# Kernel optimization log

Measured on AMD Instinct MI355X. Metric: run time of the kernel, lower is better.

Reference implementation:

```python
import jax, jax.numpy as jnp
import numpy as np

B, L, M = 64, 2048, 128  # trees, leaves per complete binary tree, mem_dim (== in_dim)


def setup_inputs() -> dict:
    key = jax.random.key(0)
    ks = jax.random.split(key, 16)
    n = lambda k, s, sc=1.0: jax.random.normal(k, s, dtype=jnp.float32) * sc
    W = 0.08  # small init scale for gate weights
    return {
        "embs": n(ks[0], (B, L, M)),
        "root_c": n(ks[1], (B, M)),
        "root_h": n(ks[2], (B, M)),
        "Wi": n(ks[3], (M, M), W), "bi": jnp.zeros((M,), jnp.float32),
        "Wf": n(ks[4], (M, M), W), "bf": jnp.zeros((M,), jnp.float32),
        "Wu": n(ks[5], (M, M), W), "bu": jnp.zeros((M,), jnp.float32),
        "Wc": n(ks[6], (M, M), W), "bc": jnp.zeros((M,), jnp.float32),
        "Wo": n(ks[7], (M, M), W), "bo": jnp.zeros((M,), jnp.float32),
    }


def reference(embs, root_c, root_h, Wi, bi, Wf, bf, Wu, bu, Wc, bc, Wo, bo):
    # Top-down binary-tree LSTM over B complete binary trees, vectorized per level.
    Bn, Ln, Mn = embs.shape
    depth = int(np.log2(Ln))  # root at level 0, leaves at level `depth`

    def composer(pc, ph):
        # BinaryTreeTopDownComposer: gates from parent hidden, cell mixes parent cell
        i = jax.nn.sigmoid(ph @ Wi + bi)
        pf = jax.nn.sigmoid(ph @ Wf + bf)
        u = jnp.tanh(ph @ Wu + bu)
        c = i * u + pf * pc
        return c, jnp.tanh(c)

    def leaf(x):
        # BinaryTreeLeafModule
        c = x @ Wc + bc
        o = jax.nn.sigmoid(x @ Wo + bo)
        return c, o * jnp.tanh(c)

    # root state comes from bp_lstm.root_c / root_h
    pc, ph = root_c[:, None, :], root_h[:, None, :]  # [B, 1, M]
    for _ in range(1, depth):  # internal levels: each node composed from its parent
        pc2 = jnp.repeat(pc, 2, axis=1)  # broadcast parent state to both children
        ph2 = jnp.repeat(ph, 2, axis=1)
        pc, ph = composer(pc2, ph2)

    # leaf level: state = cat(leaf(emb), leaf(parent_h), leaf(parent_c)) along features
    pcl = jnp.repeat(pc, 2, axis=1)  # [B, L, M]
    phl = jnp.repeat(ph, 2, axis=1)
    ce, he = leaf(embs)
    cph, hph = leaf(phl)
    cpc, hpc = leaf(pcl)
    c_leaf = jnp.concatenate([ce, cph, cpc], axis=-1)  # [B, L, 3M]
    h_leaf = jnp.concatenate([he, hph, hpc], axis=-1)  # [B, L, 3M]
    return jnp.concatenate([c_leaf, h_leaf], axis=-1)  # [B, L, 6M]
```

## Files before the change

### kernel.cpp

```cpp
#include <hip/hip_runtime.h>
#include <cstdint>
#include <cstddef>

#define Bb   64
#define Ll   2048
#define Mm   128
#define ROWS (Bb * Ll)
#define OUTC 768
#define LDA  136
#define LDF  132

typedef __attribute__((ext_vector_type(4))) float  f32x4;
typedef __attribute__((ext_vector_type(8))) short  bf16x8;
typedef __attribute__((ext_vector_type(4))) short  short4v;
typedef __bf16 bf16x8b __attribute__((ext_vector_type(8)));

__device__ __forceinline__ float rcp_(float x) {
#if __has_builtin(__builtin_amdgcn_rcpf)
    return __builtin_amdgcn_rcpf(x);
#else
    return 1.0f / x;
#endif
}
__device__ __forceinline__ float sigmoid_(float x) {
    return rcp_(1.0f + __expf(-x));
}
__device__ __forceinline__ float tanh_(float x) {
    float ax = fabsf(x);
    float r  = __expf(-2.0f * ax);
    float t  = (1.0f - r) * rcp_(1.0f + r);
    return x < 0.0f ? -t : t;
}
__device__ __forceinline__ short f2bf(float f) {
    uint32_t u = __builtin_bit_cast(uint32_t, f);
    u = (u + 0x7FFFu + ((u >> 16) & 1u)) >> 16;
    return (short)(u & 0xFFFFu);
}

__device__ __forceinline__ void lds_sync() {
    asm volatile("s_waitcnt lgkmcnt(0)\n\ts_barrier" ::: "memory");
}


__global__ __launch_bounds__(512)
void state_kernel(const float* __restrict__ root_c, const float* __restrict__ root_h,
                  const float* __restrict__ Wi, const float* __restrict__ bi,
                  const float* __restrict__ Wf, const float* __restrict__ bfv,
                  const float* __restrict__ Wu, const float* __restrict__ bu,
                  const float* __restrict__ Wc, const float* __restrict__ bc,
                  const float* __restrict__ Wo, const float* __restrict__ bo,
                  float* __restrict__ ws, short* __restrict__ wbf)
{
    const int b   = blockIdx.x;
    const int tid = threadIdx.x;
    const int m   = tid & 127;
    const int q   = tid >> 7;
    const int k0  = q * 32;

    __shared__ float h_sh[Mm];
    __shared__ float c_sh[Mm];
    __shared__ float part[4][4][Mm];

    {
        int idx  = b * 512 + tid;
        int gate = idx >> 14;
        int col  = (idx >> 7) & 127;
        int k    = idx & 127;
        const float* W = gate ? Wo : Wc;
        wbf[idx] = f2bf(W[k * Mm + col]);
    }

    float wi[32], wf[32], wu[32];
    #pragma unroll
    for (int kk = 0; kk < 32; ++kk) {
        wi[kk] = Wi[(k0 + kk) * Mm + m];
        wf[kk] = Wf[(k0 + kk) * Mm + m];
        wu[kk] = Wu[(k0 + kk) * Mm + m];
    }

    float c = 0.f;
    if (q == 0) {
        c = root_c[b * Mm + m];
        h_sh[m] = root_h[b * Mm + m];
    }
    __syncthreads();

    const float bi_m = bi[m], bf_m = bfv[m], bu_m = bu[m];

    for (int it = 0; it < 10; ++it) {
        float di0 = 0.f, di1 = 0.f, df0 = 0.f, df1 = 0.f, du0 = 0.f, du1 = 0.f;
        #pragma unroll
        for (int kk = 0; kk < 32; kk += 2) {
            float h0 = h_sh[k0 + kk], h1 = h_sh[k0 + kk + 1];
            di0 = fmaf(h0, wi[kk], di0);
            di1 = fmaf(h1, wi[kk + 1], di1);
            df0 = fmaf(h0, wf[kk], df0);
            df1 = fmaf(h1, wf[kk + 1], df1);
            du0 = fmaf(h0, wu[kk], du0);
            du1 = fmaf(h1, wu[kk + 1], du1);
        }
        part[0][q][m] = di0 + di1;
        part[1][q][m] = df0 + df1;
        part[2][q][m] = du0 + du1;
        __syncthreads();
        if (q == 0) {
            float di = (part[0][0][m] + part[0][1][m]) + (part[0][2][m] + part[0][3][m]);
            float df = (part[1][0][m] + part[1][1][m]) + (part[1][2][m] + part[1][3][m]);
            float du = (part[2][0][m] + part[2][1][m]) + (part[2][2][m] + part[2][3][m]);
            float ig = sigmoid_(di + bi_m);
            float fg = sigmoid_(df + bf_m);
            float ug = tanh_(du + bu_m);
            c = ig * ug + fg * c;
            h_sh[m] = tanh_(c);
        }
        __syncthreads();
    }
    if (q == 0) c_sh[m] = c;
    __syncthreads();

    float dch = 0.f, doh = 0.f, dcc = 0.f, doc = 0.f;
    #pragma unroll
    for (int kk = 0; kk < 32; ++kk) {
        int k = k0 + kk;
        float hk = h_sh[k], ck = c_sh[k];
        float wc = Wc[k * Mm + m], wo = Wo[k * Mm + m];
        dch = fmaf(hk, wc, dch);
        doh = fmaf(hk, wo, doh);
        dcc = fmaf(ck, wc, dcc);
        doc = fmaf(ck, wo, doc);
    }
    part[0][q][m] = dch;
    part[1][q][m] = doh;
    part[2][q][m] = dcc;
    part[3][q][m] = doc;
    __syncthreads();
    if (q == 0) {
        float Dch = (part[0][0][m] + part[0][1][m]) + (part[0][2][m] + part[0][3][m]);
        float Doh = (part[1][0][m] + part[1][1][m]) + (part[1][2][m] + part[1][3][m]);
        float Dcc = (part[2][0][m] + part[2][1][m]) + (part[2][2][m] + part[2][3][m]);
        float Doc = (part[3][0][m] + part[3][1][m]) + (part[3][2][m] + part[3][3][m]);
        const float bcm = bc[m], bom = bo[m];
        float cph = Dch + bcm;
        float cpc = Dcc + bcm;
        float hph = sigmoid_(Doh + bom) * tanh_(cph);
        float hpc = sigmoid_(Doc + bom) * tanh_(cpc);
        ws[0 * Bb * Mm + b * Mm + m] = cph;
        ws[1 * Bb * Mm + b * Mm + m] = cpc;
        ws[2 * Bb * Mm + b * Mm + m] = hph;
        ws[3 * Bb * Mm + b * Mm + m] = hpc;
    }
}

__global__ __launch_bounds__(512, 4)
void fused_kernel(const float* __restrict__ embs,
                  const short* __restrict__ wbf,
                  const float* __restrict__ bc, const float* __restrict__ bo,
                  const float* __restrict__ state,
                  float* __restrict__ out)
{
    __shared__ __align__(16) char smem[70656];
    short* A0   = (short*)smem;
    short* A1   = (short*)(smem + 17408);
    float* ce_l = (float*)(smem + 34816);
    float* he_l = (float*)(smem + 51712);
    float* st_l = (float*)(smem + 68608);

    const int tid  = threadIdx.x;
    const int w    = tid >> 6;
    const int lane = tid & 63;
    const int g    = lane >> 4;
    const int ln   = lane & 15;
    const int n0   = w * 16 + ln;
    const int rowbase0 = blockIdx.x * 128;
    const int rowbase1 = rowbase0 + 64;
    const int b        = rowbase0 >> 11;

    bf16x8 bfrag[2][4];
    #pragma unroll
    for (int gate = 0; gate < 2; ++gate)
        #pragma unroll
        for (int ks = 0; ks < 4; ++ks)
            bfrag[gate][ks] = *(const bf16x8*)(
                wbf + gate * (Mm * Mm) + n0 * Mm + ks * 32 + g * 8);
    const float biasc = bc[n0];
    const float biaso = bo[n0];
    st_l[tid] = state[(tid >> 7) * (Bb * Mm) + b * Mm + (tid & 127)];

    auto stage_load = [&](int rowbase, f32x4 (&r)[4]) {
        #pragma unroll
        for (int i = 0; i < 4; ++i) {
            int idx = tid + 512 * i;
            int rr  = idx >> 5;
            int kq  = idx & 31;
            r[i] = __builtin_nontemporal_load(
                (const f32x4*)(embs + (size_t)(rowbase + rr) * Mm + kq * 4));
        }
    };
    auto stage_write = [&](short* A, const f32x4 (&r)[4]) {
        #pragma unroll
        for (int i = 0; i < 4; ++i) {
            int idx = tid + 512 * i;
            int rr  = idx >> 5;
            int kq  = idx & 31;
            short4v s4;
            s4[0] = f2bf(r[i][0]); s4[1] = f2bf(r[i][1]);
            s4[2] = f2bf(r[i][2]); s4[3] = f2bf(r[i][3]);
            *(short4v*)(&A[rr * LDA + kq * 4]) = s4;
        }
    };
    auto do_mfma = [&](const short* A, f32x4 (&acc)[4][2]) {
        #pragma unroll
        for (int rt = 0; rt < 4; ++rt)
            #pragma unroll
            for (int gate = 0; gate < 2; ++gate) {
                float bv = gate ? biaso : biasc;
                acc[rt][gate][0] = bv; acc[rt][gate][1] = bv;
                acc[rt][gate][2] = bv; acc[rt][gate][3] = bv;
            }
        #pragma unroll
        for (int ks = 0; ks < 4; ++ks) {
            bf16x8 af[4];
            #pragma unroll
            for (int rt = 0; rt < 4; ++rt)
                af[rt] = *(const bf16x8*)(&A[(rt * 16 + ln) * LDA + ks * 32 + g * 8]);
            #pragma unroll
            for (int rt = 0; rt < 4; ++rt)
                #pragma unroll
                for (int gate = 0; gate < 2; ++gate)
                    acc[rt][gate] = __builtin_amdgcn_mfma_f32_16x16x32_bf16(
                        __builtin_bit_cast(bf16x8b, af[rt]),
                        __builtin_bit_cast(bf16x8b, bfrag[gate][ks]),
                        acc[rt][gate], 0, 0, 0);
        }
    };
    auto epilogue = [&](int rowbase, f32x4 (&acc)[4][2]) {
        #pragma unroll
        for (int half = 0; half < 2; ++half) {
            #pragma unroll
            for (int qq = 0; qq < 2; ++qq) {
                int rt = half * 2 + qq;
                #pragma unroll
                for (int r = 0; r < 4; ++r) {
                    int rowL = qq * 16 + g * 4 + r;
                    float cv = acc[rt][0][r];
                    float hv = sigmoid_(acc[rt][1][r]) * tanh_(cv);
                    ce_l[rowL * LDF + n0] = cv;
                    he_l[rowL * LDF + n0] = hv;
                }
            }
            lds_sync();
            #pragma unroll
            for (int i = 0; i < 12; ++i) {
                int u  = tid + 512 * i;
                int rg = u / 192;
                int s  = u - rg * 192;
                int sec = s >> 5;
                int cc  = s & 31;
                const float* src =
                    (sec == 0) ? (ce_l + rg * LDF + cc * 4) :
                    (sec == 3) ? (he_l + rg * LDF + cc * 4) :
                    (st_l + ((sec < 3) ? (sec - 1) : (sec - 2)) * 128 + cc * 4);
                f32x4 v = *(const f32x4*)src;
                *(f32x4*)(out + (size_t)(rowbase + half * 32 + rg) * OUTC + s * 4) = v;
            }
            lds_sync();
        }
    };

    f32x4 r0[4], r1[4];
    f32x4 acc[4][2];

    stage_load(rowbase0, r0);
    stage_write(A0, r0);
    lds_sync();

    stage_load(rowbase1, r1);

    do_mfma(A0, acc);
    stage_write(A1, r1);
    lds_sync();

    epilogue(rowbase0, acc);
    do_mfma(A1, acc);
    epilogue(rowbase1, acc);
}

extern "C" void kernel_launch(void* const* d_in, const int* in_sizes, int n_in,
                              void* d_out, int out_size, void* d_ws, size_t ws_size,
                              hipStream_t stream) {
    const float* embs   = (const float*)d_in[0];
    const float* root_c = (const float*)d_in[1];
    const float* root_h = (const float*)d_in[2];
    const float* Wi = (const float*)d_in[3];
    const float* bi = (const float*)d_in[4];
    const float* Wf = (const float*)d_in[5];
    const float* bfv= (const float*)d_in[6];
    const float* Wu = (const float*)d_in[7];
    const float* bu = (const float*)d_in[8];
    const float* Wc = (const float*)d_in[9];
    const float* bc = (const float*)d_in[10];
    const float* Wo = (const float*)d_in[11];
    const float* bo = (const float*)d_in[12];

    float* out   = (float*)d_out;
    float* state = (float*)d_ws;
    short* wbf   = (short*)d_ws + 65536;

    state_kernel<<<dim3(Bb), dim3(512), 0, stream>>>(
        root_c, root_h, Wi, bi, Wf, bfv, Wu, bu, Wc, bc, Wo, bo, state, wbf);
    fused_kernel<<<dim3(1024), dim3(512), 0, stream>>>(
        embs, wbf, bc, bo, state, out);
}
```

Before: 110.0 us.

## Load MFMA A-fragments directly from global memory, dropping LDS staging

Replaces the LDS-staged, double-buffered bf16 A tiles with direct per-lane global loads of fp32 embeddings that are converted to bf16 in registers and fed straight into the MFMA. This removes the LDS write/read traffic and one barrier, and cuts shared memory per block, which may allow more resident blocks. In exchange, all 8 waves now load the same A data redundantly from global/L2 (eightfold re-reads), the loads are less coalesced, and the explicit overlap of the next tile's load with the current MFMA is gone.

```diff
diff --git a/kernel.cpp b/kernel.cpp
--- a/kernel.cpp
+++ b/kernel.cpp
@@ -7,12 +7,10 @@
 #define Mm   128
 #define ROWS (Bb * Ll)
 #define OUTC 768
-#define LDA  136
 #define LDF  132
 
 typedef __attribute__((ext_vector_type(4))) float  f32x4;
 typedef __attribute__((ext_vector_type(8))) short  bf16x8;
-typedef __attribute__((ext_vector_type(4))) short  short4v;
 typedef __bf16 bf16x8b __attribute__((ext_vector_type(8)));
 
 __device__ __forceinline__ float rcp_(float x) {
@@ -158,12 +156,9 @@
                   const float* __restrict__ state,
                   float* __restrict__ out)
 {
-    __shared__ __align__(16) char smem[70656];
-    short* A0   = (short*)smem;
-    short* A1   = (short*)(smem + 17408);
-    float* ce_l = (float*)(smem + 34816);
-    float* he_l = (float*)(smem + 51712);
-    float* st_l = (float*)(smem + 68608);
+    __shared__ float ce_l[32 * LDF];
+    __shared__ float he_l[32 * LDF];
+    __shared__ float st_l[512];
 
     const int tid  = threadIdx.x;
     const int w    = tid >> 6;
@@ -172,7 +167,6 @@
     const int ln   = lane & 15;
     const int n0   = w * 16 + ln;
     const int rowbase0 = blockIdx.x * 128;
-    const int rowbase1 = rowbase0 + 64;
     const int b        = rowbase0 >> 11;
 
     bf16x8 bfrag[2][4];
@@ -186,53 +180,6 @@
     const float biaso = bo[n0];
     st_l[tid] = state[(tid >> 7) * (Bb * Mm) + b * Mm + (tid & 127)];
 
-    auto stage_load = [&](int rowbase, f32x4 (&r)[4]) {
-        #pragma unroll
-        for (int i = 0; i < 4; ++i) {
-            int idx = tid + 512 * i;
-            int rr  = idx >> 5;
-            int kq  = idx & 31;
-            r[i] = __builtin_nontemporal_load(
-                (const f32x4*)(embs + (size_t)(rowbase + rr) * Mm + kq * 4));
-        }
-    };
-    auto stage_write = [&](short* A, const f32x4 (&r)[4]) {
-        #pragma unroll
-        for (int i = 0; i < 4; ++i) {
-            int idx = tid + 512 * i;
-            int rr  = idx >> 5;
-            int kq  = idx & 31;
-            short4v s4;
-            s4[0] = f2bf(r[i][0]); s4[1] = f2bf(r[i][1]);
-            s4[2] = f2bf(r[i][2]); s4[3] = f2bf(r[i][3]);
-            *(short4v*)(&A[rr * LDA + kq * 4]) = s4;
-        }
-    };
-    auto do_mfma = [&](const short* A, f32x4 (&acc)[4][2]) {
-        #pragma unroll
-        for (int rt = 0; rt < 4; ++rt)
-            #pragma unroll
-            for (int gate = 0; gate < 2; ++gate) {
-                float bv = gate ? biaso : biasc;
-                acc[rt][gate][0] = bv; acc[rt][gate][1] = bv;
-                acc[rt][gate][2] = bv; acc[rt][gate][3] = bv;
-            }
-        #pragma unroll
-        for (int ks = 0; ks < 4; ++ks) {
-            bf16x8 af[4];
-            #pragma unroll
-            for (int rt = 0; rt < 4; ++rt)
-                af[rt] = *(const bf16x8*)(&A[(rt * 16 + ln) * LDA + ks * 32 + g * 8]);
-            #pragma unroll
-            for (int rt = 0; rt < 4; ++rt)
-                #pragma unroll
-                for (int gate = 0; gate < 2; ++gate)
-                    acc[rt][gate] = __builtin_amdgcn_mfma_f32_16x16x32_bf16(
-                        __builtin_bit_cast(bf16x8b, af[rt]),
-                        __builtin_bit_cast(bf16x8b, bfrag[gate][ks]),
-                        acc[rt][gate], 0, 0, 0);
-        }
-    };
     auto epilogue = [&](int rowbase, f32x4 (&acc)[4][2]) {
         #pragma unroll
         for (int half = 0; half < 2; ++half) {
@@ -267,22 +214,49 @@
         }
     };
 
-    f32x4 r0[4], r1[4];
-    f32x4 acc[4][2];
-
-    stage_load(rowbase0, r0);
-    stage_write(A0, r0);
-    lds_sync();
-
-    stage_load(rowbase1, r1);
-
-    do_mfma(A0, acc);
-    stage_write(A1, r1);
-    lds_sync();
-
-    epilogue(rowbase0, acc);
-    do_mfma(A1, acc);
-    epilogue(rowbase1, acc);
+    const float* abase = embs + (size_t)(rowbase0 + ln) * Mm + g * 8;
+
+    #pragma unroll
+    for (int t = 0; t < 2; ++t) {
+        const int rowbase = rowbase0 + t * 64;
+
+        f32x4 acc[4][2];
+        #pragma unroll
+        for (int rt = 0; rt < 4; ++rt)
+            #pragma unroll
+            for (int gate = 0; gate < 2; ++gate) {
+                float bv = gate ? biaso : biasc;
+                acc[rt][gate][0] = bv; acc[rt][gate][1] = bv;
+                acc[rt][gate][2] = bv; acc[rt][gate][3] = bv;
+            }
+
+        #pragma unroll
+        for (int ks = 0; ks < 4; ++ks) {
+            bf16x8b af[4];
+            #pragma unroll
+            for (int rt = 0; rt < 4; ++rt) {
+                const float* ap = abase + (size_t)(t * 64 + rt * 16) * Mm + ks * 32;
+                f32x4 a0 = *(const f32x4*)ap;
+                f32x4 a1 = *(const f32x4*)(ap + 4);
+                bf16x8b f;
+                f[0] = (__bf16)a0[0]; f[1] = (__bf16)a0[1];
+                f[2] = (__bf16)a0[2]; f[3] = (__bf16)a0[3];
+                f[4] = (__bf16)a1[0]; f[5] = (__bf16)a1[1];
+                f[6] = (__bf16)a1[2]; f[7] = (__bf16)a1[3];
+                af[rt] = f;
+            }
+            #pragma unroll
+            for (int rt = 0; rt < 4; ++rt)
+                #pragma unroll
+                for (int gate = 0; gate < 2; ++gate)
+                    acc[rt][gate] = __builtin_amdgcn_mfma_f32_16x16x32_bf16(
+                        af[rt],
+                        __builtin_bit_cast(bf16x8b, bfrag[gate][ks]),
+                        acc[rt][gate], 0, 0, 0);
+        }
+
+        epilogue(rowbase, acc);
+    }
 }
 
 extern "C" void kernel_launch(void* const* d_in, const int* in_sizes, int n_in,
```

After: 178.5 us. 62.3% more time.

## Fuse state recurrence into GEMM kernel with flag-based cross-block sync

Applied to the files above, without the earlier changes.

Merges the per-tree state recurrence kernel and the leaf GEMM kernel into one launch. The first 64 blocks compute the tree state, write it to workspace and publish completion through an atomic bitmask; GEMM blocks spin on the flag for their tree only before the epilogue needs it. Each block now processes 256 rows over a 4-step double-buffered loop, and weights are converted to bf16 per block from fp32 instead of through a precomputed buffer. This removes one launch and the serialization between kernels, but relies on the 512 blocks being co-resident to avoid deadlock and adds a memset launch.

```diff
diff --git a/kernel.cpp b/kernel.cpp
--- a/kernel.cpp
+++ b/kernel.cpp
@@ -31,132 +31,21 @@
     float t  = (1.0f - r) * rcp_(1.0f + r);
     return x < 0.0f ? -t : t;
 }
-__device__ __forceinline__ short f2bf(float f) {
-    uint32_t u = __builtin_bit_cast(uint32_t, f);
-    u = (u + 0x7FFFu + ((u >> 16) & 1u)) >> 16;
-    return (short)(u & 0xFFFFu);
-}
 
 __device__ __forceinline__ void lds_sync() {
     asm volatile("s_waitcnt lgkmcnt(0)\n\ts_barrier" ::: "memory");
 }
 
 
-__global__ __launch_bounds__(512)
-void state_kernel(const float* __restrict__ root_c, const float* __restrict__ root_h,
-                  const float* __restrict__ Wi, const float* __restrict__ bi,
-                  const float* __restrict__ Wf, const float* __restrict__ bfv,
-                  const float* __restrict__ Wu, const float* __restrict__ bu,
-                  const float* __restrict__ Wc, const float* __restrict__ bc,
-                  const float* __restrict__ Wo, const float* __restrict__ bo,
-                  float* __restrict__ ws, short* __restrict__ wbf)
-{
-    const int b   = blockIdx.x;
-    const int tid = threadIdx.x;
-    const int m   = tid & 127;
-    const int q   = tid >> 7;
-    const int k0  = q * 32;
-
-    __shared__ float h_sh[Mm];
-    __shared__ float c_sh[Mm];
-    __shared__ float part[4][4][Mm];
-
-    {
-        int idx  = b * 512 + tid;
-        int gate = idx >> 14;
-        int col  = (idx >> 7) & 127;
-        int k    = idx & 127;
-        const float* W = gate ? Wo : Wc;
-        wbf[idx] = f2bf(W[k * Mm + col]);
-    }
-
-    float wi[32], wf[32], wu[32];
-    #pragma unroll
-    for (int kk = 0; kk < 32; ++kk) {
-        wi[kk] = Wi[(k0 + kk) * Mm + m];
-        wf[kk] = Wf[(k0 + kk) * Mm + m];
-        wu[kk] = Wu[(k0 + kk) * Mm + m];
-    }
-
-    float c = 0.f;
-    if (q == 0) {
-        c = root_c[b * Mm + m];
-        h_sh[m] = root_h[b * Mm + m];
-    }
-    __syncthreads();
-
-    const float bi_m = bi[m], bf_m = bfv[m], bu_m = bu[m];
-
-    for (int it = 0; it < 10; ++it) {
-        float di0 = 0.f, di1 = 0.f, df0 = 0.f, df1 = 0.f, du0 = 0.f, du1 = 0.f;
-        #pragma unroll
-        for (int kk = 0; kk < 32; kk += 2) {
-            float h0 = h_sh[k0 + kk], h1 = h_sh[k0 + kk + 1];
-            di0 = fmaf(h0, wi[kk], di0);
-            di1 = fmaf(h1, wi[kk + 1], di1);
-            df0 = fmaf(h0, wf[kk], df0);
-            df1 = fmaf(h1, wf[kk + 1], df1);
-            du0 = fmaf(h0, wu[kk], du0);
-            du1 = fmaf(h1, wu[kk + 1], du1);
-        }
-        part[0][q][m] = di0 + di1;
-        part[1][q][m] = df0 + df1;
-        part[2][q][m] = du0 + du1;
-        __syncthreads();
-        if (q == 0) {
-            float di = (part[0][0][m] + part[0][1][m]) + (part[0][2][m] + part[0][3][m]);
-            float df = (part[1][0][m] + part[1][1][m]) + (part[1][2][m] + part[1][3][m]);
-            float du = (part[2][0][m] + part[2][1][m]) + (part[2][2][m] + part[2][3][m]);
-            float ig = sigmoid_(di + bi_m);
-            float fg = sigmoid_(df + bf_m);
-            float ug = tanh_(du + bu_m);
-            c = ig * ug + fg * c;
-            h_sh[m] = tanh_(c);
-        }
-        __syncthreads();
-    }
-    if (q == 0) c_sh[m] = c;
-    __syncthreads();
-
-    float dch = 0.f, doh = 0.f, dcc = 0.f, doc = 0.f;
-    #pragma unroll
-    for (int kk = 0; kk < 32; ++kk) {
-        int k = k0 + kk;
-        float hk = h_sh[k], ck = c_sh[k];
-        float wc = Wc[k * Mm + m], wo = Wo[k * Mm + m];
-        dch = fmaf(hk, wc, dch);
-        doh = fmaf(hk, wo, doh);
-        dcc = fmaf(ck, wc, dcc);
-        doc = fmaf(ck, wo, doc);
-    }
-    part[0][q][m] = dch;
-    part[1][q][m] = doh;
-    part[2][q][m] = dcc;
-    part[3][q][m] = doc;
-    __syncthreads();
-    if (q == 0) {
-        float Dch = (part[0][0][m] + part[0][1][m]) + (part[0][2][m] + part[0][3][m]);
-        float Doh = (part[1][0][m] + part[1][1][m]) + (part[1][2][m] + part[1][3][m]);
-        float Dcc = (part[2][0][m] + part[2][1][m]) + (part[2][2][m] + part[2][3][m]);
-        float Doc = (part[3][0][m] + part[3][1][m]) + (part[3][2][m] + part[3][3][m]);
-        const float bcm = bc[m], bom = bo[m];
-        float cph = Dch + bcm;
-        float cpc = Dcc + bcm;
-        float hph = sigmoid_(Doh + bom) * tanh_(cph);
-        float hpc = sigmoid_(Doc + bom) * tanh_(cpc);
-        ws[0 * Bb * Mm + b * Mm + m] = cph;
-        ws[1 * Bb * Mm + b * Mm + m] = cpc;
-        ws[2 * Bb * Mm + b * Mm + m] = hph;
-        ws[3 * Bb * Mm + b * Mm + m] = hpc;
-    }
-}
-
 __global__ __launch_bounds__(512, 4)
-void fused_kernel(const float* __restrict__ embs,
-                  const short* __restrict__ wbf,
-                  const float* __restrict__ bc, const float* __restrict__ bo,
-                  const float* __restrict__ state,
-                  float* __restrict__ out)
+void mega_kernel(const float* __restrict__ embs,
+                 const float* __restrict__ root_c, const float* __restrict__ root_h,
+                 const float* __restrict__ Wi, const float* __restrict__ bi,
+                 const float* __restrict__ Wf, const float* __restrict__ bfv,
+                 const float* __restrict__ Wu, const float* __restrict__ bu,
+                 const float* __restrict__ Wc, const float* __restrict__ bc,
+                 const float* __restrict__ Wo, const float* __restrict__ bo,
+                 float* __restrict__ ws, float* __restrict__ out)
 {
     __shared__ __align__(16) char smem[70656];
     short* A0   = (short*)smem;
@@ -164,27 +53,129 @@
     float* ce_l = (float*)(smem + 34816);
     float* he_l = (float*)(smem + 51712);
     float* st_l = (float*)(smem + 68608);
-
+    float* h_sh = (float*)smem;
+    float* c_sh = (float*)(smem + 512);
+    float* part = (float*)(smem + 1024);
+
+    unsigned long long* flag = (unsigned long long*)((char*)ws + 131072);
+
+    const int bid  = blockIdx.x;
     const int tid  = threadIdx.x;
+
+    if (bid < 64) {
+        const int b  = bid;
+        const int m  = tid & 127;
+        const int q  = tid >> 7;
+        const int k0 = q * 32;
+
+        float wi[32], wf[32], wu[32];
+        #pragma unroll
+        for (int kk = 0; kk < 32; ++kk) {
+            wi[kk] = Wi[(k0 + kk) * Mm + m];
+            wf[kk] = Wf[(k0 + kk) * Mm + m];
+            wu[kk] = Wu[(k0 + kk) * Mm + m];
+        }
+
+        float c = 0.f;
+        if (q == 0) {
+            c = root_c[b * Mm + m];
+            h_sh[m] = root_h[b * Mm + m];
+        }
+        __syncthreads();
+
+        const float bi_m = bi[m], bf_m = bfv[m], bu_m = bu[m];
+
+        for (int it = 0; it < 10; ++it) {
+            float di0 = 0.f, di1 = 0.f, df0 = 0.f, df1 = 0.f, du0 = 0.f, du1 = 0.f;
+            #pragma unroll
+            for (int kk = 0; kk < 32; kk += 2) {
+                float h0 = h_sh[k0 + kk], h1 = h_sh[k0 + kk + 1];
+                di0 = fmaf(h0, wi[kk], di0);
+                di1 = fmaf(h1, wi[kk + 1], di1);
+                df0 = fmaf(h0, wf[kk], df0);
+                df1 = fmaf(h1, wf[kk + 1], df1);
+                du0 = fmaf(h0, wu[kk], du0);
+                du1 = fmaf(h1, wu[kk + 1], du1);
+            }
+            part[(0 * 4 + q) * Mm + m] = di0 + di1;
+            part[(1 * 4 + q) * Mm + m] = df0 + df1;
+            part[(2 * 4 + q) * Mm + m] = du0 + du1;
+            __syncthreads();
+            if (q == 0) {
+                float di = (part[0 * Mm + m] + part[1 * Mm + m]) + (part[2 * Mm + m] + part[3 * Mm + m]);
+                float df = (part[4 * Mm + m] + part[5 * Mm + m]) + (part[6 * Mm + m] + part[7 * Mm + m]);
+                float du = (part[8 * Mm + m] + part[9 * Mm + m]) + (part[10 * Mm + m] + part[11 * Mm + m]);
+                float ig = sigmoid_(di + bi_m);
+                float fg = sigmoid_(df + bf_m);
+                float ug = tanh_(du + bu_m);
+                c = ig * ug + fg * c;
+                h_sh[m] = tanh_(c);
+            }
+            __syncthreads();
+        }
+        if (q == 0) c_sh[m] = c;
+        __syncthreads();
+
+        float dch = 0.f, doh = 0.f, dcc = 0.f, doc = 0.f;
+        #pragma unroll
+        for (int kk = 0; kk < 32; ++kk) {
+            int k = k0 + kk;
+            float hk = h_sh[k], ck = c_sh[k];
+            float wc = Wc[k * Mm + m], wo = Wo[k * Mm + m];
+            dch = fmaf(hk, wc, dch);
+            doh = fmaf(hk, wo, doh);
+            dcc = fmaf(ck, wc, dcc);
+            doc = fmaf(ck, wo, doc);
+        }
+        part[(0 * 4 + q) * Mm + m] = dch;
+        part[(1 * 4 + q) * Mm + m] = doh;
+        part[(2 * 4 + q) * Mm + m] = dcc;
+        part[(3 * 4 + q) * Mm + m] = doc;
+        __syncthreads();
+        if (q == 0) {
+            float Dch = (part[0 * Mm + m] + part[1 * Mm + m]) + (part[2 * Mm + m] + part[3 * Mm + m]);
+            float Doh = (part[4 * Mm + m] + part[5 * Mm + m]) + (part[6 * Mm + m] + part[7 * Mm + m]);
+            float Dcc = (part[8 * Mm + m] + part[9 * Mm + m]) + (part[10 * Mm + m] + part[11 * Mm + m]);
+            float Doc = (part[12 * Mm + m] + part[13 * Mm + m]) + (part[14 * Mm + m] + part[15 * Mm + m]);
+            const float bcm = bc[m], bom = bo[m];
+            float cph = Dch + bcm;
+            float cpc = Dcc + bcm;
+            float hph = sigmoid_(Doh + bom) * tanh_(cph);
+            float hpc = sigmoid_(Doc + bom) * tanh_(cpc);
+            ws[0 * Bb * Mm + b * Mm + m] = cph;
+            ws[1 * Bb * Mm + b * Mm + m] = cpc;
+            ws[2 * Bb * Mm + b * Mm + m] = hph;
+            ws[3 * Bb * Mm + b * Mm + m] = hpc;
+        }
+        __syncthreads();
+        __threadfence();
+        if (tid == 0) atomicOr(flag, 1ull << b);
+        __syncthreads();
+    }
+
     const int w    = tid >> 6;
     const int lane = tid & 63;
     const int g    = lane >> 4;
     const int ln   = lane & 15;
     const int n0   = w * 16 + ln;
-    const int rowbase0 = blockIdx.x * 128;
-    const int rowbase1 = rowbase0 + 64;
-    const int b        = rowbase0 >> 11;
-
-    bf16x8 bfrag[2][4];
+    const int rows0 = bid * 256;
+    const int b     = rows0 >> 11;
+
+    bf16x8b bfrag[2][4];
     #pragma unroll
-    for (int gate = 0; gate < 2; ++gate)
-        #pragma unroll
-        for (int ks = 0; ks < 4; ++ks)
-            bfrag[gate][ks] = *(const bf16x8*)(
-                wbf + gate * (Mm * Mm) + n0 * Mm + ks * 32 + g * 8);
+    for (int gate = 0; gate < 2; ++gate) {
+        const float* W = gate ? Wo : Wc;
+        #pragma unroll
+        for (int ks = 0; ks < 4; ++ks) {
+            bf16x8b f;
+            #pragma unroll
+            for (int j = 0; j < 8; ++j)
+                f[j] = (__bf16)W[(ks * 32 + g * 8 + j) * Mm + n0];
+            bfrag[gate][ks] = f;
+        }
+    }
     const float biasc = bc[n0];
     const float biaso = bo[n0];
-    st_l[tid] = state[(tid >> 7) * (Bb * Mm) + b * Mm + (tid & 127)];
 
     auto stage_load = [&](int rowbase, f32x4 (&r)[4]) {
         #pragma unroll
@@ -203,8 +194,10 @@
             int rr  = idx >> 5;
             int kq  = idx & 31;
             short4v s4;
-            s4[0] = f2bf(r[i][0]); s4[1] = f2bf(r[i][1]);
-            s4[2] = f2bf(r[i][2]); s4[3] = f2bf(r[i][3]);
+            s4[0] = (short)__builtin_bit_cast(unsigned short, (__bf16)r[i][0]);
+            s4[1] = (short)__builtin_bit_cast(unsigned short, (__bf16)r[i][1]);
+            s4[2] = (short)__builtin_bit_cast(unsigned short, (__bf16)r[i][2]);
+            s4[3] = (short)__builtin_bit_cast(unsigned short, (__bf16)r[i][3]);
             *(short4v*)(&A[rr * LDA + kq * 4]) = s4;
         }
     };
@@ -229,7 +222,7 @@
                 for (int gate = 0; gate < 2; ++gate)
                     acc[rt][gate] = __builtin_amdgcn_mfma_f32_16x16x32_bf16(
                         __builtin_bit_cast(bf16x8b, af[rt]),
-                        __builtin_bit_cast(bf16x8b, bfrag[gate][ks]),
+                        bfrag[gate][ks],
                         acc[rt][gate], 0, 0, 0);
         }
     };
@@ -267,22 +260,38 @@
         }
     };
 
-    f32x4 r0[4], r1[4];
+    f32x4 r[4];
     f32x4 acc[4][2];
 
-    stage_load(rowbase0, r0);
-    stage_write(A0, r0);
+    stage_load(rows0, r);
+    stage_write(A0, r);
     lds_sync();
 
-    stage_load(rowbase1, r1);
-
-    do_mfma(A0, acc);
-    stage_write(A1, r1);
-    lds_sync();
-
-    epilogue(rowbase0, acc);
-    do_mfma(A1, acc);
-    epilogue(rowbase1, acc);
+    for (int t = 0; t < 4; ++t) {
+        short* Acur = (t & 1) ? A1 : A0;
+        short* Anxt = (t & 1) ? A0 : A1;
+
+        if (t < 3) stage_load(rows0 + (t + 1) * 64, r);
+        do_mfma(Acur, acc);
+        if (t < 3) stage_write(Anxt, r);
+
+        if (t == 0) {
+            if (tid == 0) {
+                while (!(__hip_atomic_load(flag, __ATOMIC_ACQUIRE,
+                                           __HIP_MEMORY_SCOPE_AGENT) >> b & 1ull))
+                    __builtin_amdgcn_s_sleep(16);
+            }
+            lds_sync();
+            {
+                unsigned int u = __hip_atomic_load(
+                    (const unsigned int*)ws + (tid >> 7) * (Bb * Mm) + b * Mm + (tid & 127),
+                    __ATOMIC_RELAXED, __HIP_MEMORY_SCOPE_AGENT);
+                st_l[tid] = __builtin_bit_cast(float, u);
+            }
+        }
+
+        epilogue(rows0 + t * 64, acc);
+    }
 }
 
 extern "C" void kernel_launch(void* const* d_in, const int* in_sizes, int n_in,
@@ -303,11 +312,10 @@
     const float* bo = (const float*)d_in[12];
 
     float* out   = (float*)d_out;
-    float* state = (float*)d_ws;
-    short* wbf   = (short*)d_ws + 65536;
-
-    state_kernel<<<dim3(Bb), dim3(512), 0, stream>>>(
-        root_c, root_h, Wi, bi, Wf, bfv, Wu, bu, Wc, bc, Wo, bo, state, wbf);
-    fused_kernel<<<dim3(1024), dim3(512), 0, stream>>>(
-        embs, wbf, bc, bo, state, out);
-}
+    float* ws    = (float*)d_ws;
+
+    hipMemsetAsync((char*)d_ws + 131072, 0, 8, stream);
+
+    mega_kernel<<<dim3(512), dim3(512), 0, stream>>>(
+        embs, root_c, root_h, Wi, bi, Wf, bfv, Wu, bu, Wc, bc, Wo, bo, ws, out);
+}
```

New measurement: 149.2 us. 1.36x slower.
